# Kernel tuning notes

Measured on AMD Instinct MI355X. Metric: run time of the kernel, lower is better.

## Reference

```python
import jax, jax.numpy as jnp
import numpy as np

B, S, D = 4, 2048, 1024


def setup_inputs() -> dict:
    key = jax.random.key(0)
    ks = jax.random.split(key, 9)
    scale = 1.0 / np.sqrt(D)
    x = jax.random.normal(ks[0], (B, S, D), dtype=jnp.float32)
    mask = jnp.tril(jnp.ones((S, S), dtype=jnp.int32))[None, :, :]  # causal, broadcast over batch
    Wq = jax.random.normal(ks[1], (D, D), dtype=jnp.float32) * scale
    bq = jax.random.normal(ks[2], (D,), dtype=jnp.float32) * 0.01
    Wk = jax.random.normal(ks[3], (D, D), dtype=jnp.float32) * scale
    bk = jax.random.normal(ks[4], (D,), dtype=jnp.float32) * 0.01
    Wv = jax.random.normal(ks[5], (D, D), dtype=jnp.float32) * scale
    bv = jax.random.normal(ks[6], (D,), dtype=jnp.float32) * 0.01
    Wo = jax.random.normal(ks[7], (D, D), dtype=jnp.float32) * scale
    bo = jax.random.normal(ks[8], (D,), dtype=jnp.float32) * 0.01
    return {"x": x, "mask": mask, "Wq": Wq, "bq": bq, "Wk": Wk, "bk": bk,
            "Wv": Wv, "bv": bv, "Wo": Wo, "bo": bo}


def reference(x, mask, Wq, bq, Wk, bk, Wv, bv, Wo, bo):
    # Linear projections (torch Linear: x @ W^T + b; here W stored as [in, out])
    Q = jnp.einsum('bsd,de->bse', x, Wq) + bq
    K = jnp.einsum('bsd,de->bse', x, Wk) + bk
    V = jnp.einsum('bsd,de->bse', x, Wv) + bv
    d_k = Q.shape[-1]
    scores = jnp.einsum('bqd,bkd->bqk', Q, K) / jnp.sqrt(jnp.float32(d_k))
    scores = jnp.where(mask == 0, jnp.float32(-jnp.inf), scores)
    attn_weights = jax.nn.softmax(scores, axis=-1)  # [B, S, S]
    attn_output = jnp.einsum('bqk,bkd->bqd', attn_weights, V)
    output = jnp.einsum('bsd,de->bse', attn_output, Wo) + bo
    return output, attn_weights
```

## Files before the change

kernel.cpp:

```cpp
#include <hip/hip_runtime.h>
#include <cstdint>
#include <cstddef>
#include <cmath>

typedef __bf16 bf16_t;
typedef bf16_t bf16x8 __attribute__((ext_vector_type(8)));
typedef bf16_t bf16x4 __attribute__((ext_vector_type(4)));
typedef float f32x4 __attribute__((ext_vector_type(4)));

constexpr int kB = 4;
constexpr int kS = 2048;
constexpr int kD = 1024;
constexpr int BM = 128, BN = 128, BK = 32;
constexpr int TILE_ELEMS = (BM + BN) * BK;

typedef __attribute__((address_space(1))) void as1void;
typedef __attribute__((address_space(3))) void as3void;

__device__ __forceinline__ void gload16(const void* g, void* l) {
  __builtin_amdgcn_global_load_lds((as1void*)g, (as3void*)l, 16, 0, 0);
}

__device__ __forceinline__ void wgbar() {
  asm volatile("" ::: "memory");
  __builtin_amdgcn_s_barrier();
  asm volatile("" ::: "memory");
}

__device__ __forceinline__ void gemm_mainloop(
    const bf16_t* __restrict__ A, int lda,
    const bf16_t* __restrict__ B, int ldb,
    int ksteps, bf16_t* lds, f32x4 acc[4][4]) {
  const int tid = threadIdx.x;
  const int w = tid >> 6, lane = tid & 63;
  const int srow = lane >> 2;
  const int scol = (lane & 3) << 3;
  const int wr = (w >> 1) << 6, wc = (w & 1) << 6;
  const int fr = lane & 15, kg = lane >> 4;

  const bf16_t* ga0 = A + (size_t)(w * 16 + srow) * lda + scol;
  const bf16_t* ga1 = A + (size_t)(64 + w * 16 + srow) * lda + scol;
  const bf16_t* gb0 = B + (size_t)(w * 16 + srow) * ldb + scol;
  const bf16_t* gb1 = B + (size_t)(64 + w * 16 + srow) * ldb + scol;
  const int oa0 = (w * 16) * BK;
  const int oa1 = (64 + w * 16) * BK;
  const int ob0 = BM * BK + (w * 16) * BK;
  const int ob1 = BM * BK + (64 + w * 16) * BK;

  gload16(ga0, lds + oa0);
  gload16(ga1, lds + oa1);
  gload16(gb0, lds + ob0);
  gload16(gb1, lds + ob1);
  ga0 += BK; ga1 += BK; gb0 += BK; gb1 += BK;
  __syncthreads();

  int cur = 0;
  for (int ks = 0; ks < ksteps; ++ks) {
    const int nxt = cur ^ 1;
    if (ks + 1 < ksteps) {
      bf16_t* nb = lds + nxt * TILE_ELEMS;
      gload16(ga0, nb + oa0);
      gload16(ga1, nb + oa1);
      gload16(gb0, nb + ob0);
      gload16(gb1, nb + ob1);
      ga0 += BK; ga1 += BK; gb0 += BK; gb1 += BK;
    }
    const bf16_t* cb = lds + cur * TILE_ELEMS;
    bf16x8 af[4], bfv[4];
#pragma unroll
    for (int m = 0; m < 4; ++m)
      af[m] = *(const bf16x8*)(cb + (wr + m * 16 + fr) * BK + kg * 8);
#pragma unroll
    for (int n = 0; n < 4; ++n)
      bfv[n] = *(const bf16x8*)(cb + BM * BK + (wc + n * 16 + fr) * BK + kg * 8);
#pragma unroll
    for (int m = 0; m < 4; ++m)
#pragma unroll
      for (int n = 0; n < 4; ++n)
        acc[m][n] = __builtin_amdgcn_mfma_f32_16x16x32_bf16(af[m], bfv[n],
                                                            acc[m][n], 0, 0, 0);
    __syncthreads();
    cur = nxt;
  }
}

__device__ __forceinline__ void gemm256_loop(
    const bf16_t* __restrict__ A, int lda,
    const bf16_t* __restrict__ B, int ldb,
    int nk, bf16_t* lds, f32x4 acc[8][4]) {
  const int tid = threadIdx.x;
  const int wid = tid >> 6, lane = tid & 63;
  const int wm = wid >> 2, wn = wid & 3;
  const int fr = lane & 15, kg = (lane >> 4) & 3;
  const int s_row = ((tid >> 7) << 4) | (tid & 15);
  const int s_col = ((tid >> 4) & 7) << 3;
  const bf16_t* pA = A + (size_t)s_row * lda + s_col;
  const bf16_t* pB = B + (size_t)s_row * ldb + s_col;
  const int ldst = wid << 9;

  auto stg = [&](int tt, int op, int h, int j) {
    const bf16_t* g = (op ? pB : pA) + (size_t)(h * 128 + j * 64) * (op ? ldb : lda)
                      + (size_t)tt * 64;
    bf16_t* d = lds + (((tt & 1) * 4 + op * 2 + h) * 8192) + j * 4096 + ldst;
    gload16(g, d);
  };

#pragma unroll
  for (int h = 0; h < 2; ++h)
#pragma unroll
    for (int j = 0; j < 2; ++j) { stg(0, 0, h, j); stg(0, 1, h, j); }
  stg(1, 1, 0, 0); stg(1, 1, 0, 1); stg(1, 1, 1, 0); stg(1, 1, 1, 1);
  stg(1, 0, 0, 0); stg(1, 0, 1, 0);
  asm volatile("s_waitcnt vmcnt(6)" ::: "memory");
  wgbar();

  const int arow = kg * 128 + fr * 8;
  for (int t = 0; t < nk; ++t) {
    const bf16_t* sb = lds + (t & 1) * 32768;
    const bf16_t* aslot = sb + wm * 8192;
    const bf16_t* bslot = sb + (2 + (wn >> 1)) * 8192 + (wn & 1) * 4096;
    bf16x8 bF[4][2];
#pragma unroll
    for (int q = 0; q < 4; ++q) {
      bf16x8 aF[2][2];
#pragma unroll
      for (int mi = 0; mi < 2; ++mi)
#pragma unroll
        for (int ks = 0; ks < 2; ++ks)
          aF[mi][ks] = *(const bf16x8*)(aslot + (2 * q + mi) * 1024 + ks * 512 + arow);
      if (q == 0) {
#pragma unroll
        for (int n = 0; n < 4; ++n)
#pragma unroll
          for (int ks = 0; ks < 2; ++ks)
            bF[n][ks] = *(const bf16x8*)(bslot + n * 1024 + ks * 512 + arow);
      }
      if (q == 0)      { if (t + 1 <= nk - 1) { stg(t + 1, 0, 0, 1); stg(t + 1, 0, 1, 1); } }
      else if (q == 1) { if (t + 2 <= nk - 1) { stg(t + 2, 1, 0, 0); stg(t + 2, 1, 0, 1); } }
      else if (q == 2) { if (t + 2 <= nk - 1) { stg(t + 2, 1, 1, 0); stg(t + 2, 1, 1, 1); } }
      else             { if (t + 2 <= nk - 1) { stg(t + 2, 0, 0, 0); stg(t + 2, 0, 1, 0); } }
      wgbar();
      __builtin_amdgcn_s_setprio(1);
#pragma unroll
      for (int mi = 0; mi < 2; ++mi)
#pragma unroll
        for (int n = 0; n < 4; ++n)
#pragma unroll
          for (int ks = 0; ks < 2; ++ks)
            acc[2 * q + mi][n] = __builtin_amdgcn_mfma_f32_16x16x32_bf16(
                aF[mi][ks], bF[n][ks], acc[2 * q + mi][n], 0, 0, 0);
      __builtin_amdgcn_s_setprio(0);
      asm volatile("s_waitcnt lgkmcnt(0)" ::: "memory");
      if (q == 3 && t < nk - 1) {
        if (t + 2 <= nk - 1) asm volatile("s_waitcnt vmcnt(6)" ::: "memory");
        else                 asm volatile("s_waitcnt vmcnt(0)" ::: "memory");
      }
      wgbar();
    }
  }
}


__global__ __launch_bounds__(512, 2)
void k_qk256(const bf16_t* __restrict__ A, const bf16_t* __restrict__ WT,
             const float* __restrict__ bq, const float* __restrict__ bk,
             bf16_t* __restrict__ Qb, bf16_t* __restrict__ Kb) {
  __shared__ bf16_t lds[65536];
  const int id = blockIdx.x;
  const int swz = (id & 7) * 32 + (id >> 3);
  const int mb = swz >> 3, nb = swz & 7;
  const int m0 = mb * 256, n0 = nb * 256;
  f32x4 acc[8][4] = {};
  gemm256_loop(A + (size_t)m0 * kD, kD, WT + (size_t)n0 * kD, kD,
               kD / 64, lds, acc);
  const int lane = threadIdx.x & 63, wid = threadIdx.x >> 6;
  const int wm = wid >> 2, wn = wid & 3, fr = lane & 15, kgr = lane >> 4;
  const int which = n0 >> 10;
  bf16_t* C = which == 0 ? Qb : Kb;
  const float* bias = which == 0 ? bq : bk;
#pragma unroll
  for (int n = 0; n < 4; ++n) {
    const int col = (n0 & 1023) + wn * 64 + n * 16 + fr;
    const float bvv = bias[col];
#pragma unroll
    for (int m = 0; m < 8; ++m)
#pragma unroll
      for (int i = 0; i < 4; ++i) {
        const int row = m0 + wm * 128 + m * 16 + kgr * 4 + i;
        C[(size_t)row * kD + col] = (bf16_t)(acc[m][n][i] + bvv);
      }
  }
}

__global__ __launch_bounds__(256)
void k_v128(const bf16_t* __restrict__ A, const bf16_t* __restrict__ Bw,
            const float* __restrict__ bias, bf16_t* __restrict__ VT) {
  __shared__ bf16_t lds[2 * TILE_ELEMS];
  const int id = blockIdx.x;
  const int swz = (id & 7) * 64 + (id >> 3);
  const int m0 = (swz >> 3) * BM, n0 = (swz & 7) * BN;
  f32x4 acc[4][4] = {};
  gemm_mainloop(A + (size_t)m0 * kD, kD, Bw + (size_t)n0 * kD, kD, kD / BK, lds, acc);
  const int tid = threadIdx.x, w = tid >> 6, lane = tid & 63;
  const int wr = (w >> 1) << 6, wc = (w & 1) << 6, fr = lane & 15, kg = lane >> 4;
#pragma unroll
  for (int n = 0; n < 4; ++n) {
    const int col = n0 + wc + n * 16 + fr;
    const float bvv = bias[col];
#pragma unroll
    for (int m = 0; m < 4; ++m)
#pragma unroll
      for (int i = 0; i < 4; ++i) {
        const int row = m0 + wr + m * 16 + kg * 4 + i;
        const int b = row >> 11, s = row & (kS - 1);
        VT[((size_t)b * kD + col) * kS + s] = (bf16_t)(acc[m][n][i] + bvv);
      }
  }
}

__global__ __launch_bounds__(256)
void k_gemm_scores(const bf16_t* __restrict__ Q, const bf16_t* __restrict__ K,
                   float* __restrict__ Sc) {
  const int t = blockIdx.x, b = blockIdx.y;
  int by = (int)((sqrtf(8.f * t + 1.f) - 1.f) * 0.5f);
  while ((by + 1) * (by + 2) / 2 <= t) ++by;
  while (by * (by + 1) / 2 > t) --by;
  const int bx = t - by * (by + 1) / 2;
  __shared__ bf16_t lds[2 * TILE_ELEMS];
  const int m0 = by * BM, n0 = bx * BN;
  f32x4 acc[4][4] = {};
  gemm_mainloop(Q + (size_t)b * kS * kD + (size_t)m0 * kD, kD,
                K + (size_t)b * kS * kD + (size_t)n0 * kD, kD, kD / BK, lds, acc);
  float* Sb = Sc + (size_t)b * kS * kS;
  const int tid = threadIdx.x, w = tid >> 6, lane = tid & 63;
  const int wr = (w >> 1) << 6, wc = (w & 1) << 6, fr = lane & 15, kg = lane >> 4;
#pragma unroll
  for (int m = 0; m < 4; ++m)
#pragma unroll
    for (int n = 0; n < 4; ++n)
#pragma unroll
      for (int i = 0; i < 4; ++i) {
        const int row = m0 + wr + m * 16 + kg * 4 + i;
        const int col = n0 + wc + n * 16 + fr;
        Sb[(size_t)row * kS + col] = acc[m][n][i] * 0.03125f;
      }
}

__global__ __launch_bounds__(256)
void k_softmax(float* __restrict__ P, bf16_t* __restrict__ Pb) {
  const int row = blockIdx.x;
  const int q = row & (kS - 1);
  float* p = P + (size_t)row * kS;
  bf16_t* pb = Pb + (size_t)row * kS;
  const int L = q + 1;
  __shared__ float buf[kS];
  __shared__ float red[8];
  const int tid = threadIdx.x;
  float4* b4 = (float4*)buf;
  const float4* p4 = (const float4*)p;
  if (tid * 4 < L) b4[tid] = p4[tid];
  if (1024 + tid * 4 < L) b4[tid + 256] = p4[tid + 256];
  __syncthreads();
  float mx = -1e30f;
  for (int k = tid; k < L; k += 256) mx = fmaxf(mx, buf[k]);
#pragma unroll
  for (int s2 = 32; s2 >= 1; s2 >>= 1) mx = fmaxf(mx, __shfl_xor(mx, s2));
  if ((tid & 63) == 0) red[tid >> 6] = mx;
  __syncthreads();
  mx = fmaxf(fmaxf(red[0], red[1]), fmaxf(red[2], red[3]));
  float sm = 0.f;
  for (int k = tid; k < L; k += 256) {
    const float e = __expf(buf[k] - mx);
    buf[k] = e;
    sm += e;
  }
#pragma unroll
  for (int s2 = 32; s2 >= 1; s2 >>= 1) sm += __shfl_xor(sm, s2);
  if ((tid & 63) == 0) red[4 + (tid >> 6)] = sm;
  __syncthreads();
  const float inv = 1.f / (red[4] + red[5] + red[6] + red[7]);
  for (int k = tid; k < L; k += 256) {
    const float v = buf[k] * inv;
    p[k] = v;
    pb[k] = (bf16_t)v;
  }
  for (int k = L + tid; k < kS; k += 256) {
    p[k] = 0.f;
    pb[k] = (bf16_t)0.f;
  }
}

__global__ __launch_bounds__(256)
void k_gemm_pv(const bf16_t* __restrict__ P, const bf16_t* __restrict__ VT,
               bf16_t* __restrict__ AO) {
  const int bx = blockIdx.x, b = blockIdx.z;
  const int by = (int)gridDim.y - 1 - (int)blockIdx.y;
  __shared__ bf16_t lds[2 * TILE_ELEMS];
  const int m0 = by * BM, n0 = bx * BN;
  const int ksteps = (m0 + BM) / BK;
  f32x4 acc[4][4] = {};
  gemm_mainloop(P + (size_t)b * kS * kS + (size_t)m0 * kS, kS,
                VT + (size_t)b * kD * kS + (size_t)n0 * kS, kS, ksteps, lds, acc);
  bf16_t* AOb = AO + (size_t)b * kS * kD;
  const int tid = threadIdx.x, w = tid >> 6, lane = tid & 63;
  const int wr = (w >> 1) << 6, wc = (w & 1) << 6, fr = lane & 15, kg = lane >> 4;
#pragma unroll
  for (int m = 0; m < 4; ++m)
#pragma unroll
    for (int n = 0; n < 4; ++n)
#pragma unroll
      for (int i = 0; i < 4; ++i) {
        const int row = m0 + wr + m * 16 + kg * 4 + i;
        const int col = n0 + wc + n * 16 + fr;
        AOb[(size_t)row * kD + col] = (bf16_t)acc[m][n][i];
      }
}

__global__ __launch_bounds__(256)
void k_gemm_out(const bf16_t* __restrict__ A, const bf16_t* __restrict__ Bw,
                const float* __restrict__ bias, float* __restrict__ C) {
  __shared__ bf16_t lds[2 * TILE_ELEMS];
  const int id = blockIdx.x;
  const int swz = (id & 7) * 64 + (id >> 3);
  const int m0 = (swz >> 3) * BM, n0 = (swz & 7) * BN;
  f32x4 acc[4][4] = {};
  gemm_mainloop(A + (size_t)m0 * kD, kD, Bw + (size_t)n0 * kD, kD, kD / BK, lds, acc);
  const int tid = threadIdx.x, w = tid >> 6, lane = tid & 63;
  const int wr = (w >> 1) << 6, wc = (w & 1) << 6, fr = lane & 15, kg = lane >> 4;
#pragma unroll
  for (int n = 0; n < 4; ++n) {
    const int col = n0 + wc + n * 16 + fr;
    const float bv = bias[col];
#pragma unroll
    for (int m = 0; m < 4; ++m)
#pragma unroll
      for (int i = 0; i < 4; ++i) {
        const int row = m0 + wr + m * 16 + kg * 4 + i;
        C[(size_t)row * kD + col] = acc[m][n][i] + bv;
      }
  }
}

__global__ __launch_bounds__(256)
void k_prep(const float* __restrict__ X, bf16_t* __restrict__ Y,
            const float* __restrict__ W0, const float* __restrict__ W1,
            const float* __restrict__ W2, const float* __restrict__ W3,
            bf16_t* __restrict__ T0, bf16_t* __restrict__ T1,
            bf16_t* __restrict__ T2, bf16_t* __restrict__ T3) {
  const int tx = threadIdx.x & 31, ty = threadIdx.x >> 5;
  if (blockIdx.z == 4) {
    const size_t n4 = (size_t)kB * kS * kD / 4;
    size_t i = ((size_t)blockIdx.y * 32 + blockIdx.x) * 256 + threadIdx.x;
    const size_t stride = (size_t)1024 * 256;
    const float4* X4 = (const float4*)X;
    bf16x4* Y4 = (bf16x4*)Y;
    for (; i < n4; i += stride) {
      const float4 v = X4[i];
      bf16x4 o = {(bf16_t)v.x, (bf16_t)v.y, (bf16_t)v.z, (bf16_t)v.w};
      Y4[i] = o;
    }
    return;
  }
  const float* W = blockIdx.z == 0 ? W0 : blockIdx.z == 1 ? W1 : blockIdx.z == 2 ? W2 : W3;
  bf16_t* T = blockIdx.z == 0 ? T0 : blockIdx.z == 1 ? T1 : blockIdx.z == 2 ? T2 : T3;
  __shared__ float t[32][33];
  const int x0 = blockIdx.x * 32, y0 = blockIdx.y * 32;
#pragma unroll
  for (int j = 0; j < 4; ++j)
    t[ty + 8 * j][tx] = W[(size_t)(y0 + ty + 8 * j) * kD + x0 + tx];
  __syncthreads();
#pragma unroll
  for (int j = 0; j < 4; ++j)
    T[(size_t)(x0 + ty + 8 * j) * kD + y0 + tx] = (bf16_t)t[tx][ty + 8 * j];
}

extern "C" void kernel_launch(void* const* d_in, const int* in_sizes, int n_in,
                              void* d_out, int out_size, void* d_ws, size_t ws_size,
                              hipStream_t stream) {
  (void)in_sizes; (void)n_in; (void)out_size; (void)ws_size;
  const float* x  = (const float*)d_in[0];
  const float* Wq = (const float*)d_in[2];
  const float* bq = (const float*)d_in[3];
  const float* Wk = (const float*)d_in[4];
  const float* bk = (const float*)d_in[5];
  const float* Wv = (const float*)d_in[6];
  const float* bv = (const float*)d_in[7];
  const float* Wo = (const float*)d_in[8];
  const float* bo = (const float*)d_in[9];

  float* out  = (float*)d_out;
  float* Pout = out + (size_t)kB * kS * kD;

  bf16_t* WqT = (bf16_t*)d_ws;
  bf16_t* WkT = WqT + (size_t)kD * kD;
  bf16_t* WvT = WkT + (size_t)kD * kD;
  bf16_t* WoT = WvT + (size_t)kD * kD;
  bf16_t* Qb  = WoT + (size_t)kD * kD;
  bf16_t* Kb  = Qb + (size_t)kB * kS * kD;
  bf16_t* VTb = Kb + (size_t)kB * kS * kD;
  bf16_t* Pb  = VTb + (size_t)kB * kS * kD;
  bf16_t* AOb = Pb + (size_t)kB * kS * kS;
  bf16_t* xb  = AOb + (size_t)kB * kS * kD;

  k_prep<<<dim3(32, 32, 5), 256, 0, stream>>>(x, xb, Wq, Wk, Wv, Wo,
                                              WqT, WkT, WvT, WoT);
  k_qk256<<<256, 512, 0, stream>>>(xb, WqT, bq, bk, Qb, Kb);
  k_v128<<<512, 256, 0, stream>>>(xb, WvT, bv, VTb);
  k_gemm_scores<<<dim3(136, kB), 256, 0, stream>>>(Qb, Kb, Pout);
  k_softmax<<<kB * kS, 256, 0, stream>>>(Pout, Pb);
  k_gemm_pv<<<dim3(8, 16, kB), 256, 0, stream>>>(Pb, VTb, AOb);
  k_gemm_out<<<512, 256, 0, stream>>>(AOb, WoT, bo, out);
}
```

Before: 220.9 us.

## Merge V projection into scores kernel and trim bf16 zero-fill to band

```diff
diff --git a/kernel.cpp b/kernel.cpp
--- a/kernel.cpp
+++ b/kernel.cpp
@@ -193,57 +193,56 @@
 }
 
 __global__ __launch_bounds__(256)
-void k_v128(const bf16_t* __restrict__ A, const bf16_t* __restrict__ Bw,
-            const float* __restrict__ bias, bf16_t* __restrict__ VT) {
+void k_scores_v(const bf16_t* __restrict__ Q, const bf16_t* __restrict__ K,
+                float* __restrict__ Sc,
+                const bf16_t* __restrict__ X, const bf16_t* __restrict__ WvT,
+                const float* __restrict__ bv, bf16_t* __restrict__ VT) {
   __shared__ bf16_t lds[2 * TILE_ELEMS];
   const int id = blockIdx.x;
-  const int swz = (id & 7) * 64 + (id >> 3);
-  const int m0 = (swz >> 3) * BM, n0 = (swz & 7) * BN;
-  f32x4 acc[4][4] = {};
-  gemm_mainloop(A + (size_t)m0 * kD, kD, Bw + (size_t)n0 * kD, kD, kD / BK, lds, acc);
   const int tid = threadIdx.x, w = tid >> 6, lane = tid & 63;
   const int wr = (w >> 1) << 6, wc = (w & 1) << 6, fr = lane & 15, kg = lane >> 4;
-#pragma unroll
-  for (int n = 0; n < 4; ++n) {
-    const int col = n0 + wc + n * 16 + fr;
-    const float bvv = bias[col];
+  if (id < 544) {
+    const int b = id / 136, t = id % 136;
+    int by = (int)((sqrtf(8.f * t + 1.f) - 1.f) * 0.5f);
+    while ((by + 1) * (by + 2) / 2 <= t) ++by;
+    while (by * (by + 1) / 2 > t) --by;
+    const int bx = t - by * (by + 1) / 2;
+    const int m0 = by * BM, n0 = bx * BN;
+    f32x4 acc[4][4] = {};
+    gemm_mainloop(Q + (size_t)b * kS * kD + (size_t)m0 * kD, kD,
+                  K + (size_t)b * kS * kD + (size_t)n0 * kD, kD, kD / BK, lds, acc);
+    float* Sb = Sc + (size_t)b * kS * kS;
 #pragma unroll
     for (int m = 0; m < 4; ++m)
 #pragma unroll
-      for (int i = 0; i < 4; ++i) {
-        const int row = m0 + wr + m * 16 + kg * 4 + i;
-        const int b = row >> 11, s = row & (kS - 1);
-        VT[((size_t)b * kD + col) * kS + s] = (bf16_t)(acc[m][n][i] + bvv);
-      }
-  }
-}
-
-__global__ __launch_bounds__(256)
-void k_gemm_scores(const bf16_t* __restrict__ Q, const bf16_t* __restrict__ K,
-                   float* __restrict__ Sc) {
-  const int t = blockIdx.x, b = blockIdx.y;
-  int by = (int)((sqrtf(8.f * t + 1.f) - 1.f) * 0.5f);
-  while ((by + 1) * (by + 2) / 2 <= t) ++by;
-  while (by * (by + 1) / 2 > t) --by;
-  const int bx = t - by * (by + 1) / 2;
-  __shared__ bf16_t lds[2 * TILE_ELEMS];
-  const int m0 = by * BM, n0 = bx * BN;
-  f32x4 acc[4][4] = {};
-  gemm_mainloop(Q + (size_t)b * kS * kD + (size_t)m0 * kD, kD,
-                K + (size_t)b * kS * kD + (size_t)n0 * kD, kD, kD / BK, lds, acc);
-  float* Sb = Sc + (size_t)b * kS * kS;
-  const int tid = threadIdx.x, w = tid >> 6, lane = tid & 63;
-  const int wr = (w >> 1) << 6, wc = (w & 1) << 6, fr = lane & 15, kg = lane >> 4;
-#pragma unroll
-  for (int m = 0; m < 4; ++m)
-#pragma unroll
-    for (int n = 0; n < 4; ++n)
-#pragma unroll
-      for (int i = 0; i < 4; ++i) {
-        const int row = m0 + wr + m * 16 + kg * 4 + i;
-        const int col = n0 + wc + n * 16 + fr;
-        Sb[(size_t)row * kS + col] = acc[m][n][i] * 0.03125f;
-      }
+      for (int n = 0; n < 4; ++n)
+#pragma unroll
+        for (int i = 0; i < 4; ++i) {
+          const int row = m0 + wr + m * 16 + kg * 4 + i;
+          const int col = n0 + wc + n * 16 + fr;
+          Sb[(size_t)row * kS + col] = acc[m][n][i] * 0.03125f;
+        }
+  } else {
+    const int vid = id - 544;
+    const int swz = (vid & 7) * 64 + (vid >> 3);
+    const int m0 = (swz >> 3) * BM, n0 = (swz & 7) * BN;
+    f32x4 acc[4][4] = {};
+    gemm_mainloop(X + (size_t)m0 * kD, kD, WvT + (size_t)n0 * kD, kD,
+                  kD / BK, lds, acc);
+#pragma unroll
+    for (int n = 0; n < 4; ++n) {
+      const int col = n0 + wc + n * 16 + fr;
+      const float bvv = bv[col];
+#pragma unroll
+      for (int m = 0; m < 4; ++m)
+#pragma unroll
+        for (int i = 0; i < 4; ++i) {
+          const int row = m0 + wr + m * 16 + kg * 4 + i;
+          const int b = row >> 11, s = row & (kS - 1);
+          VT[((size_t)b * kD + col) * kS + s] = (bf16_t)(acc[m][n][i] + bvv);
+        }
+    }
+  }
 }
 
 __global__ __launch_bounds__(256)
@@ -284,10 +283,9 @@
     p[k] = v;
     pb[k] = (bf16_t)v;
   }
-  for (int k = L + tid; k < kS; k += 256) {
-    p[k] = 0.f;
-    pb[k] = (bf16_t)0.f;
-  }
+  for (int k = L + tid; k < kS; k += 256) p[k] = 0.f;
+  const int bandEnd = (q & ~127) + 128;
+  for (int k = L + tid; k < bandEnd; k += 256) pb[k] = (bf16_t)0.f;
 }
 
 __global__ __launch_bounds__(256)
@@ -405,8 +403,7 @@
   k_prep<<<dim3(32, 32, 5), 256, 0, stream>>>(x, xb, Wq, Wk, Wv, Wo,
                                               WqT, WkT, WvT, WoT);
   k_qk256<<<256, 512, 0, stream>>>(xb, WqT, bq, bk, Qb, Kb);
-  k_v128<<<512, 256, 0, stream>>>(xb, WvT, bv, VTb);
-  k_gemm_scores<<<dim3(136, kB), 256, 0, stream>>>(Qb, Kb, Pout);
+  k_scores_v<<<1056, 256, 0, stream>>>(Qb, Kb, Pout, xb, WvT, bv, VTb);
   k_softmax<<<kB * kS, 256, 0, stream>>>(Pout, Pb);
   k_gemm_pv<<<dim3(8, 16, kB), 256, 0, stream>>>(Pb, VTb, AOb);
   k_gemm_out<<<512, 256, 0, stream>>>(AOb, WoT, bo, out);
```

After: 209.6 us. 5.1% less time.
